# Performance work log

Hardware: AMD Instinct MI355X
Metric: run time of the kernel (lower is better)

The kernel has to match this reference:

```python
import jax, jax.numpy as jnp
import numpy as np

NUM_HEADS = 16
DIM_HEAD = 64
SCALE = DIM_HEAD ** -0.5
ROPE_BASE = 10000.0


def _rope(t):
    # t: [b, h, n, d] -> rotary embedding with rotate-half convention
    n, d = t.shape[2], t.shape[3]
    inv_freq = 1.0 / (ROPE_BASE ** (jnp.arange(0, d, 2, dtype=jnp.float32) / d))
    freqs = jnp.arange(n, dtype=jnp.float32)[:, None] * inv_freq[None, :]  # [n, d/2]
    cos = jnp.concatenate([jnp.cos(freqs), jnp.cos(freqs)], axis=-1)  # [n, d]
    sin = jnp.concatenate([jnp.sin(freqs), jnp.sin(freqs)], axis=-1)
    t1, t2 = jnp.split(t, 2, axis=-1)
    rot = jnp.concatenate([-t2, t1], axis=-1)
    return t * cos + rot * sin


def setup_inputs() -> dict:
    key = jax.random.key(0)
    k1, k2, k3 = jax.random.split(key, 3)
    B, N, D = 2, 2049, 1024  # 2048 patches + 1 cls token
    x = jax.random.normal(k1, (B, N, D), dtype=jnp.float32)
    ln_gamma = jnp.ones((D,), dtype=jnp.float32)
    ln_beta = jnp.zeros((D,), dtype=jnp.float32)
    w_qkv = jax.random.normal(k2, (D, 3 * NUM_HEADS * DIM_HEAD), dtype=jnp.float32) * 0.02
    w_out = jax.random.normal(k3, (NUM_HEADS * DIM_HEAD, D), dtype=jnp.float32) * 0.02
    return {"x": x, "ln_gamma": ln_gamma, "ln_beta": ln_beta, "w_qkv": w_qkv, "w_out": w_out}


def reference(x, ln_gamma, ln_beta, w_qkv, w_out):
    B, N, D = x.shape
    # LayerNorm (eps=1e-5, torch default)
    mu = jnp.mean(x, axis=-1, keepdims=True)
    var = jnp.mean(jnp.square(x - mu), axis=-1, keepdims=True)
    xn = (x - mu) * jax.lax.rsqrt(var + 1e-5) * ln_gamma + ln_beta
    # QKV projection (no bias)
    qkv = xn @ w_qkv  # [B, N, 3*H*Dh]
    q, k, v = jnp.split(qkv, 3, axis=-1)
    def to_heads(t):
        return t.reshape(B, N, NUM_HEADS, DIM_HEAD).transpose(0, 2, 1, 3)  # [B,H,N,Dh]
    q, k, v = to_heads(q), to_heads(k), to_heads(v)
    # cls token excluded from RoPE
    q = jnp.concatenate([q[:, :, :1, :], _rope(q[:, :, 1:, :])], axis=2)
    k = jnp.concatenate([k[:, :, :1, :], _rope(k[:, :, 1:, :])], axis=2)
    dots = jnp.einsum('bhqd,bhkd->bhqk', q, k) * SCALE
    attn = jax.nn.softmax(dots, axis=-1)
    out = jnp.einsum('bhqk,bhkd->bhqd', attn, v)
    out = out.transpose(0, 2, 1, 3).reshape(B, N, NUM_HEADS * DIM_HEAD)
    return out @ w_out
```

## Files before the change

### kernel.cpp

```cpp
#include <hip/hip_runtime.h>

#define B_    2
#define N_    2049
#define NPAD  2112
#define D_    1024
#define H_    16
#define DH    64
#define MROWS (B_ * N_)
#define MPAD  4224
#define QSCALE 0.18033688011117674f

using bf16x8 = __attribute__((ext_vector_type(8))) short;
using f32x4  = __attribute__((ext_vector_type(4))) float;
using f32x16 = __attribute__((ext_vector_type(16))) float;

#define AS1 __attribute__((address_space(1)))
#define AS3 __attribute__((address_space(3)))

__device__ __forceinline__ float bf2f(short s) {
  union { unsigned u; float f; } a; a.u = ((unsigned)(unsigned short)s) << 16; return a.f;
}
__device__ __forceinline__ short f2bf(float f) {
  union { float f; unsigned u; } a; a.f = f;
  unsigned r = a.u + 0x7fffu + ((a.u >> 16) & 1u);
  return (short)(r >> 16);
}
__device__ __forceinline__ float hexp2(float x) { return __builtin_amdgcn_exp2f(x); }
__device__ __forceinline__ void dma16(const short* g, AS3 short* l) {
  __builtin_amdgcn_global_load_lds((const AS1 unsigned*)g, (AS3 unsigned*)l, 16, 0, 0);
}

__device__ __forceinline__ size_t tiled_off(int m, int k) {
  return ((size_t)(m >> 7) << 17)
       + (size_t)(((k >> 5) << 12)
       + ((((m & 127) >> 4)) << 9)
       + (((((m & 15) << 2) | ((k & 31) >> 3))) << 3)
       + (k & 7));
}

__global__ __launch_bounds__(256) void prep_kernel(const float* __restrict__ x,
                                                   const float* __restrict__ gamma,
                                                   const float* __restrict__ beta,
                                                   short* __restrict__ xn,
                                                   const float* __restrict__ w_qkv,
                                                   short* __restrict__ wqkvT,
                                                   const float* __restrict__ w_out,
                                                   short* __restrict__ woutT) {
  int blk = blockIdx.x;
  int tid = threadIdx.x;
  __shared__ float T[64][65];
  __shared__ float sb[4], s2b[4];

  if (blk < MROWS) {
    int row = blk;
    int b = row >= N_;
    int rowp = b * NPAD + (row - b * N_);
    const float4 v = ((const float4*)(x + (size_t)row * D_))[tid];
    float s  = v.x + v.y + v.z + v.w;
    float ss = v.x * v.x + v.y * v.y + v.z * v.z + v.w * v.w;
    for (int o = 1; o < 64; o <<= 1) { s += __shfl_xor(s, o, 64); ss += __shfl_xor(ss, o, 64); }
    int wid = tid >> 6;
    if ((tid & 63) == 0) { sb[wid] = s; s2b[wid] = ss; }
    __syncthreads();
    float st  = sb[0] + sb[1] + sb[2] + sb[3];
    float sst = s2b[0] + s2b[1] + s2b[2] + s2b[3];
    float mu  = st * (1.0f / D_);
    float var = sst * (1.0f / D_) - mu * mu;
    float rs  = rsqrtf(var + 1e-5f);
    const float4 g  = ((const float4*)gamma)[tid];
    const float4 be = ((const float4*)beta)[tid];
    short4 o4;
    o4.x = f2bf((v.x - mu) * rs * g.x + be.x);
    o4.y = f2bf((v.y - mu) * rs * g.y + be.y);
    o4.z = f2bf((v.z - mu) * rs * g.z + be.z);
    o4.w = f2bf((v.w - mu) * rs * g.w + be.w);
    *(short4*)(xn + tiled_off(rowp, tid * 4)) = o4;
    return;
  }

  const float* in; short* out; int Nn, t2;
  int b2 = blk - MROWS;
  if (b2 < 768) { in = w_qkv; out = wqkvT; Nn = 3072; t2 = b2; }
  else          { in = w_out; out = woutT; Nn = 1024; t2 = b2 - 768; }
  int k0 = (t2 & 15) * 64;
  int n0 = (t2 >> 4) * 64;
  int r = tid >> 2, c0 = (tid & 3) * 16;
  const float* ip = in + (size_t)(k0 + r) * Nn + n0 + c0;
  #pragma unroll
  for (int j = 0; j < 4; ++j) {
    float4 v = *(const float4*)(ip + j * 4);
    T[r][c0 + j * 4 + 0] = v.x; T[r][c0 + j * 4 + 1] = v.y;
    T[r][c0 + j * 4 + 2] = v.z; T[r][c0 + j * 4 + 3] = v.w;
  }
  __syncthreads();
  bf16x8 w0, w1;
  #pragma unroll
  for (int j = 0; j < 8; ++j) {
    w0[j] = f2bf(T[c0 + j][r]);
    w1[j] = f2bf(T[c0 + 8 + j][r]);
  }
  *(bf16x8*)(out + tiled_off(n0 + r, k0 + c0))     = w0;
  *(bf16x8*)(out + tiled_off(n0 + r, k0 + c0 + 8)) = w1;
}

#define BM 128
#define BK 32
__global__ __launch_bounds__(256) void gemm_qkv_rope(const short* __restrict__ A,
                                                     const short* __restrict__ BT,
                                                     short* __restrict__ qg,
                                                     short* __restrict__ kfrag,
                                                     short* __restrict__ vfrag) {
  int lane = threadIdx.x & 63, wid = threadIdx.x >> 6;
  int quad = lane >> 4, l16 = lane & 15;
  int wr = wid >> 1, wc = wid & 1;
  int chunk = gridDim.x >> 3;
  int swz = (blockIdx.x & 7) * chunk + (blockIdx.x >> 3);
  int mb = swz % 33, nb = swz / 33;
  int m0 = mb * BM;
  int n0 = nb * BM;

  __shared__ __align__(16) short pool[17408];
  AS3 short* AbufL = (AS3 short*)pool;
  AS3 short* BbufL = (AS3 short*)(pool + 8192);
  const short* AbufR = pool;
  const short* BbufR = pool + 8192;

  f32x4 acc[4][4] = {};

  const short* Ap = A  + ((size_t)(m0 >> 7) << 17);
  const short* Bp = BT + ((size_t)(n0 >> 7) << 17);

  auto stage = [&](int kt, int bb) {
    #pragma unroll
    for (int i = 0; i < 2; ++i) {
      int j = wid * 2 + i;
      dma16(Ap + ((size_t)kt << 12) + j * 512 + lane * 8, AbufL + bb * 4096 + j * 512);
      dma16(Bp + ((size_t)kt << 12) + j * 512 + lane * 8, BbufL + bb * 4096 + j * 512);
    }
  };

  stage(0, 0);
  __syncthreads();

  for (int kt = 0; kt < 32; ++kt) {
    int cur = kt & 1;
    if (kt + 1 < 32) stage(kt + 1, cur ^ 1);
    const short* Ab = AbufR + cur * 4096;
    const short* Bb = BbufR + cur * 4096;
    bf16x8 af[4], bfr[4];
    #pragma unroll
    for (int s = 0; s < 4; ++s)
      af[s] = *(const bf16x8*)&Ab[(wr * 64 + s * 16 + l16) * BK + quad * 8];
    #pragma unroll
    for (int t = 0; t < 4; ++t)
      bfr[t] = *(const bf16x8*)&Bb[(wc * 64 + t * 16 + l16) * BK + quad * 8];
    #pragma unroll
    for (int s = 0; s < 4; ++s)
      #pragma unroll
      for (int t = 0; t < 4; ++t)
        acc[s][t] = __builtin_amdgcn_mfma_f32_16x16x32_bf16(af[s], bfr[t], acc[s][t], 0, 0, 0);
    __syncthreads();
  }

  short* Ct = pool;
  #pragma unroll
  for (int s = 0; s < 4; ++s)
    #pragma unroll
    for (int t = 0; t < 4; ++t) {
      int col = wc * 64 + t * 16 + l16;
      #pragma unroll
      for (int r = 0; r < 4; ++r) {
        int row = wr * 64 + s * 16 + quad * 4 + r;
        Ct[row * 136 + col] = f2bf(acc[s][t][r]);
      }
    }
  __syncthreads();

  int third = nb >> 3;
  int hpair = (nb & 7) * 2;
  int tid = threadIdx.x;

  if (third == 0) {
    int p = tid & 3, nl = tid >> 2;
    #pragma unroll
    for (int tt = 0; tt < 2; ++tt) {
      int rl = tt * 64 + nl;
      int rg = m0 + rl;
      int b = rg >= NPAD;
      int n = rg - b * NPAD;
      bool valid = n < N_;
      bool rot = valid && n > 0;
      float csv[8], snv[8];
      #pragma unroll
      for (int j = 0; j < 8; ++j) {
        int i = p * 8 + j;
        float ang = rot ? (float)(n - 1) * hexp2((float)i * -0.4152410118609203f) : 0.0f;
        float rev = ang * 0.15915494309189535f;
        rev = rev - floorf(rev);
        snv[j] = rot ? __builtin_amdgcn_sinf(rev) : 0.0f;
        csv[j] = rot ? __builtin_amdgcn_cosf(rev) : 1.0f;
      }
      #pragma unroll
      for (int hh = 0; hh < 2; ++hh) {
        bf16x8 w1v = {}, w2v = {};
        if (valid) {
          bf16x8 va = *(const bf16x8*)&Ct[rl * 136 + hh * 64 + p * 8];
          bf16x8 vb = *(const bf16x8*)&Ct[rl * 136 + hh * 64 + p * 8 + 32];
          #pragma unroll
          for (int j = 0; j < 8; ++j) {
            float a = bf2f(va[j]), b2 = bf2f(vb[j]);
            w1v[j] = f2bf((a * csv[j] - b2 * snv[j]) * QSCALE);
            w2v[j] = f2bf((b2 * csv[j] + a * snv[j]) * QSCALE);
          }
        }
        size_t ob = ((size_t)(b * 16 + hpair + hh) * NPAD + n) * DH;
        *(bf16x8*)(qg + ob + p * 8)      = w1v;
        *(bf16x8*)(qg + ob + 32 + p * 8) = w2v;
      }
    }
  } else if (third == 1) {
    int rl = tid & 127, hi = tid >> 7;
    int rg = m0 + rl;
    int b = rg >= NPAD;
    int n = rg - b * NPAD;
    bool valid = n < N_;
    bool rot = valid && n > 0;
    int kt = n >> 6, g = (n >> 5) & 1, lk = n & 31;
    int l = hi * 32 + lk;
    #pragma unroll
    for (int s2 = 0; s2 < 2; ++s2) {
      float csv[8], snv[8];
      #pragma unroll
      for (int j = 0; j < 8; ++j) {
        int i = s2 * 16 + hi * 8 + j;
        float ang = rot ? (float)(n - 1) * hexp2((float)i * -0.4152410118609203f) : 0.0f;
        float rev = ang * 0.15915494309189535f;
        rev = rev - floorf(rev);
        snv[j] = rot ? __builtin_amdgcn_sinf(rev) : 0.0f;
        csv[j] = rot ? __builtin_amdgcn_cosf(rev) : 1.0f;
      }
      #pragma unroll
      for (int hh = 0; hh < 2; ++hh) {
        bf16x8 wlo = {}, whi = {};
        if (valid) {
          bf16x8 va = *(const bf16x8*)&Ct[rl * 136 + hh * 64 + s2 * 16 + hi * 8];
          bf16x8 vb = *(const bf16x8*)&Ct[rl * 136 + hh * 64 + s2 * 16 + hi * 8 + 32];
          #pragma unroll
          for (int j = 0; j < 8; ++j) {
            float a = bf2f(va[j]), b2 = bf2f(vb[j]);
            wlo[j] = f2bf(a * csv[j] - b2 * snv[j]);
            whi[j] = f2bf(b2 * csv[j] + a * snv[j]);
          }
        }
        short* base = kfrag + (size_t)(b * 16 + hpair + hh) * NPAD * DH + (size_t)kt * 4096;
        *(bf16x8*)(base + (g * 4 + s2) * 512 + l * 8)     = wlo;
        *(bf16x8*)(base + (g * 4 + s2 + 2) * 512 + l * 8) = whi;
      }
    }
  } else {
    int lk = tid & 31, z = tid >> 5;
    #pragma unroll
    for (int oo = 0; oo < 2; ++oo) {
      int o = z * 2 + oo;
      int rg = m0 + o * 8;
      int b = rg >= NPAD;
      int n0o = rg - b * NPAD;
      int kt = n0o >> 6;
      int s = (n0o >> 4) & 3;
      int hi = (n0o >> 3) & 1;
      #pragma unroll
      for (int hh = 0; hh < 2; ++hh) {
        short* base = vfrag + (size_t)(b * 16 + hpair + hh) * NPAD * DH + (size_t)kt * 4096;
        #pragma unroll
        for (int m = 0; m < 2; ++m) {
          bf16x8 wv = {};
          #pragma unroll
          for (int j = 0; j < 8; ++j)
            if (n0o + j < N_) wv[j] = Ct[(o * 8 + j) * 136 + hh * 64 + m * 32 + lk];
          *(bf16x8*)(base + (m * 4 + s) * 512 + (hi * 32 + lk) * 8) = wv;
        }
      }
    }
  }
}

template <typename OutT>
__global__ __launch_bounds__(256) void gemm128(const short* __restrict__ A,
                                               const short* __restrict__ BT,
                                               OutT* __restrict__ C,
                                               int Mstore, int Ncols, int K) {
  int lane = threadIdx.x & 63, wid = threadIdx.x >> 6;
  int quad = lane >> 4, l16 = lane & 15;
  int wr = wid >> 1, wc = wid & 1;
  int chunk = gridDim.x >> 3;
  int swz = (blockIdx.x & 7) * chunk + (blockIdx.x >> 3);
  int mb = swz % 33, nb = swz / 33;
  int m0 = mb * BM;
  int n0 = nb * BM;

  __shared__ __align__(16) short Abuf[2][BM * BK];
  __shared__ __align__(16) short Bbuf[2][BM * BK];
  AS3 short* AbufL = (AS3 short*)&Abuf[0][0];
  AS3 short* BbufL = (AS3 short*)&Bbuf[0][0];

  f32x4 acc[4][4] = {};

  const short* Ap = A  + ((size_t)(m0 >> 7) << 17);
  const short* Bp = BT + ((size_t)(n0 >> 7) << 17);

  auto stage = [&](int kt, int bb) {
    #pragma unroll
    for (int i = 0; i < 2; ++i) {
      int j = wid * 2 + i;
      dma16(Ap + ((size_t)kt << 12) + j * 512 + lane * 8, AbufL + bb * (BM * BK) + j * 512);
      dma16(Bp + ((size_t)kt << 12) + j * 512 + lane * 8, BbufL + bb * (BM * BK) + j * 512);
    }
  };

  stage(0, 0);
  __syncthreads();

  int KT = K / BK;
  for (int kt = 0; kt < KT; ++kt) {
    int cur = kt & 1;
    if (kt + 1 < KT) stage(kt + 1, cur ^ 1);
    const short* Ab = &Abuf[cur][0];
    const short* Bb = &Bbuf[cur][0];
    bf16x8 af[4], bfr[4];
    #pragma unroll
    for (int s = 0; s < 4; ++s)
      af[s] = *(const bf16x8*)&Ab[(wr * 64 + s * 16 + l16) * BK + quad * 8];
    #pragma unroll
    for (int t = 0; t < 4; ++t)
      bfr[t] = *(const bf16x8*)&Bb[(wc * 64 + t * 16 + l16) * BK + quad * 8];
    #pragma unroll
    for (int s = 0; s < 4; ++s)
      #pragma unroll
      for (int t = 0; t < 4; ++t)
        acc[s][t] = __builtin_amdgcn_mfma_f32_16x16x32_bf16(af[s], bfr[t], acc[s][t], 0, 0, 0);
    __syncthreads();
  }

  #pragma unroll
  for (int s = 0; s < 4; ++s)
    #pragma unroll
    for (int r = 0; r < 4; ++r) {
      int row = m0 + wr * 64 + s * 16 + quad * 4 + r;
      if (row < Mstore) {
        size_t rb = (size_t)row * Ncols + n0 + wc * 64;
        #pragma unroll
        for (int t = 0; t < 4; ++t) {
          float val = acc[s][t][r];
          if constexpr (sizeof(OutT) == 2)
            C[rb + t * 16 + l16] = (OutT)(unsigned short)f2bf(val);
          else
            C[rb + t * 16 + l16] = (OutT)val;
        }
      }
    }
}

__global__ __launch_bounds__(256, 3) void attn_kernel(const short* __restrict__ qg,
                                                      const short* __restrict__ kfrag,
                                                      const short* __restrict__ vfrag,
                                                      short* __restrict__ out) {
  int blk = blockIdx.x;
  int xcd = blk & 7;
  int t_  = blk >> 3;
  int bh  = xcd * 4 + (t_ & 3);
  int qblk = t_ >> 2;
  int b = bh >> 4, h = bh & 15;

  int lane = threadIdx.x & 63, wid = threadIdx.x >> 6;
  int q    = lane & 31;
  int half = lane >> 5;
  int q0   = qblk * 128 + wid * 32;
  size_t hb = (size_t)bh * NPAD * DH;
  const short* kf_hb = kfrag + hb;
  const short* vf_hb = vfrag + hb;

  __shared__ __align__(16) short Kbuf[3][4096];
  __shared__ __align__(16) short Vbuf[3][4096];
  AS3 short* KbufL = (AS3 short*)&Kbuf[0][0];
  AS3 short* VbufL = (AS3 short*)&Vbuf[0][0];
  const short* KbufR = &Kbuf[0][0];
  const short* VbufR = &Vbuf[0][0];

  int qr = q0 + q; if (qr >= NPAD) qr = 0;
  const short* qp = qg + hb + (size_t)qr * DH + half * 8;
  bf16x8 qf[4];
  #pragma unroll
  for (int s = 0; s < 4; ++s) qf[s] = *(const bf16x8*)(qp + s * 16);

  f32x16 o0 = {}, o1 = {};
  float lrun = 0.0f;

  auto stage = [&](int kt, int bb) {
    const short* ksrc = kf_hb + (size_t)kt * 4096;
    const short* vsrc = vf_hb + (size_t)kt * 4096;
    #pragma unroll
    for (int i = 0; i < 2; ++i) {
      int j = wid * 2 + i;
      dma16(ksrc + j * 512 + lane * 8, KbufL + bb * 4096 + j * 512);
      dma16(vsrc + j * 512 + lane * 8, VbufL + bb * 4096 + j * 512);
    }
  };

  stage(0, 0);
  stage(1, 1);

  #define NKT 33
  for (int kt = 0; kt < NKT; ++kt) {
    int rb = kt % 3;
    int k0 = kt * 64;

    if (kt == NKT - 1) asm volatile("s_waitcnt vmcnt(0)" ::: "memory");
    else               asm volatile("s_waitcnt vmcnt(4)" ::: "memory");
    __builtin_amdgcn_s_barrier();

    if (kt + 2 < NKT) stage(kt + 2, (kt + 2) % 3);
    __builtin_amdgcn_sched_barrier(0);

    const short* Vc = VbufR + rb * 4096;
    bf16x8 vf0[4], vf1[4];
    #pragma unroll
    for (int s = 0; s < 4; ++s) {
      vf0[s] = *(const bf16x8*)&Vc[(0 * 4 + s) * 512 + lane * 8];
      vf1[s] = *(const bf16x8*)&Vc[(4 + s) * 512 + lane * 8];
    }

    const short* Kc = KbufR + rb * 4096;
    f32x16 sA = {}, sB = {};
    __builtin_amdgcn_s_setprio(1);
    #pragma unroll
    for (int s = 0; s < 4; ++s) {
      bf16x8 kf0 = *(const bf16x8*)&Kc[(0 * 4 + s) * 512 + lane * 8];
      bf16x8 kf1 = *(const bf16x8*)&Kc[(1 * 4 + s) * 512 + lane * 8];
      sA = __builtin_amdgcn_mfma_f32_32x32x16_bf16(kf0, qf[s], sA, 0, 0, 0);
      sB = __builtin_amdgcn_mfma_f32_32x32x16_bf16(kf1, qf[s], sB, 0, 0, 0);
    }
    __builtin_amdgcn_s_setprio(0);

    if (k0 + 64 > N_) {
      #pragma unroll
      for (int rr = 0; rr < 16; ++rr) {
        int key = (rr & 3) + 8 * (rr >> 2) + 4 * half;
        if (k0 + key >= N_)      sA[rr] = -1e30f;
        if (k0 + 32 + key >= N_) sB[rr] = -1e30f;
      }
    }

    float vsum = 0.0f;
    #pragma unroll
    for (int rr = 0; rr < 16; ++rr) {
      sA[rr] = hexp2(sA[rr]); vsum += sA[rr];
      sB[rr] = hexp2(sB[rr]); vsum += sB[rr];
    }
    lrun += vsum;

    unsigned w[4][4];
    #pragma unroll
    for (int g = 0; g < 2; ++g) {
      #pragma unroll
      for (int fs = 0; fs < 2; ++fs) {
        int b0 = fs * 8;
        float e0, e1, e2, e3, e4, e5, e6, e7;
        if (g == 0) {
          e0 = sA[b0+0]; e1 = sA[b0+1]; e2 = sA[b0+2]; e3 = sA[b0+3];
          e4 = sA[b0+4]; e5 = sA[b0+5]; e6 = sA[b0+6]; e7 = sA[b0+7];
        } else {
          e0 = sB[b0+0]; e1 = sB[b0+1]; e2 = sB[b0+2]; e3 = sB[b0+3];
          e4 = sB[b0+4]; e5 = sB[b0+5]; e6 = sB[b0+6]; e7 = sB[b0+7];
        }
        unsigned X1, X2, Y1, Y2;
        asm("v_cvt_pk_bf16_f32 %0, %1, %2" : "=v"(X1) : "v"(e0), "v"(e1));
        asm("v_cvt_pk_bf16_f32 %0, %1, %2" : "=v"(X2) : "v"(e2), "v"(e3));
        asm("v_cvt_pk_bf16_f32 %0, %1, %2" : "=v"(Y1) : "v"(e4), "v"(e5));
        asm("v_cvt_pk_bf16_f32 %0, %1, %2" : "=v"(Y2) : "v"(e6), "v"(e7));
        asm("v_permlane32_swap_b32 %0, %1" : "+v"(X1), "+v"(Y1));
        asm("v_permlane32_swap_b32 %0, %1" : "+v"(X2), "+v"(Y2));
        int kst = g * 2 + fs;
        w[kst][0] = X1; w[kst][1] = X2; w[kst][2] = Y1; w[kst][3] = Y2;
      }
    }

    __builtin_amdgcn_s_setprio(1);
    #pragma unroll
    for (int kst = 0; kst < 4; ++kst) {
      union { unsigned u[4]; bf16x8 v; } bw;
      bw.u[0] = w[kst][0]; bw.u[1] = w[kst][1]; bw.u[2] = w[kst][2]; bw.u[3] = w[kst][3];
      o0 = __builtin_amdgcn_mfma_f32_32x32x16_bf16(vf0[kst], bw.v, o0, 0, 0, 0);
      o1 = __builtin_amdgcn_mfma_f32_32x32x16_bf16(vf1[kst], bw.v, o1, 0, 0, 0);
    }
    __builtin_amdgcn_s_setprio(0);
  }

  lrun += __shfl_xor(lrun, 32, 64);

  int qrow = q0 + q;
  if (qrow < N_) {
    float inv = 1.0f / lrun;
    int grow = b * N_ + qrow;
    #pragma unroll
    for (int m = 0; m < 2; ++m) {
      #pragma unroll
      for (int gq = 0; gq < 4; ++gq) {
        float a0 = (m ? o1[gq*4+0] : o0[gq*4+0]) * inv;
        float a1 = (m ? o1[gq*4+1] : o0[gq*4+1]) * inv;
        float a2 = (m ? o1[gq*4+2] : o0[gq*4+2]) * inv;
        float a3 = (m ? o1[gq*4+3] : o0[gq*4+3]) * inv;
        short4 st;
        st.x = f2bf(a0); st.y = f2bf(a1); st.z = f2bf(a2); st.w = f2bf(a3);
        int dh = m * 32 + gq * 8 + half * 4;
        *(short4*)(out + tiled_off(grow, h * DH + dh)) = st;
      }
    }
  }
}

extern "C" void kernel_launch(void* const* d_in, const int* in_sizes, int n_in,
                              void* d_out, int out_size, void* d_ws, size_t ws_size,
                              hipStream_t stream) {
  const float* x     = (const float*)d_in[0];
  const float* gamma = (const float*)d_in[1];
  const float* beta  = (const float*)d_in[2];
  const float* w_qkv = (const float*)d_in[3];
  const float* w_out = (const float*)d_in[4];

  short* wqkvT = (short*)d_ws;
  short* woutT = wqkvT + (size_t)3072 * 1024;
  short* xn    = woutT + (size_t)1024 * 1024;
  short* qg    = xn    + (size_t)MPAD * 1024;
  short* kfragG = qg    + (size_t)B_ * H_ * NPAD * DH;
  short* vfragG = kfragG + (size_t)B_ * H_ * NPAD * DH;
  short* attn_out = xn;

  prep_kernel<<<MROWS + 768 + 256, 256, 0, stream>>>(x, gamma, beta, xn,
                                                     w_qkv, wqkvT, w_out, woutT);
  gemm_qkv_rope<<<792, 256, 0, stream>>>(xn, wqkvT, qg, kfragG, vfragG);
  attn_kernel<<<544, 256, 0, stream>>>(qg, kfragG, vfragG, attn_out);
  gemm128<float><<<264, 256, 0, stream>>>(attn_out, woutT, (float*)d_out, MROWS, 1024, 1024);
}
```

Before: 209.9 us.

## Halve attention and out-projection tile sizes to double block counts

The attention kernel now uses 2-wave blocks covering 64 queries each (1056 blocks instead of 544), and drops from triple to double buffering of K/V tiles with a full vmcnt(0) wait each step. The output projection becomes a specialized 64x128-tile GEMM with 528 blocks instead of 264 blocks of 128x128. Both changes aim to fill the GPU's compute units better and cut tail imbalance. In exchange, K/V reuse per block drops, so more global/L2 traffic, and the shallower prefetch pipeline may expose load latency.

```diff
diff --git a/kernel.cpp b/kernel.cpp
--- a/kernel.cpp
+++ b/kernel.cpp
@@ -284,57 +284,55 @@
   }
 }
 
-template <typename OutT>
-__global__ __launch_bounds__(256) void gemm128(const short* __restrict__ A,
-                                               const short* __restrict__ BT,
-                                               OutT* __restrict__ C,
-                                               int Mstore, int Ncols, int K) {
+__global__ __launch_bounds__(256) void gemm_out(const short* __restrict__ A,
+                                                const short* __restrict__ BT,
+                                                float* __restrict__ C) {
   int lane = threadIdx.x & 63, wid = threadIdx.x >> 6;
   int quad = lane >> 4, l16 = lane & 15;
   int wr = wid >> 1, wc = wid & 1;
   int chunk = gridDim.x >> 3;
   int swz = (blockIdx.x & 7) * chunk + (blockIdx.x >> 3);
-  int mb = swz % 33, nb = swz / 33;
-  int m0 = mb * BM;
-  int n0 = nb * BM;
-
-  __shared__ __align__(16) short Abuf[2][BM * BK];
-  __shared__ __align__(16) short Bbuf[2][BM * BK];
+  int mb = swz % 66, nb = swz / 66;
+  int m0 = mb * 64;
+  int n0 = nb * 128;
+
+  __shared__ __align__(16) short Abuf[2][2048];
+  __shared__ __align__(16) short Bbuf[2][4096];
   AS3 short* AbufL = (AS3 short*)&Abuf[0][0];
   AS3 short* BbufL = (AS3 short*)&Bbuf[0][0];
 
-  f32x4 acc[4][4] = {};
+  f32x4 acc[2][4] = {};
 
   const short* Ap = A  + ((size_t)(m0 >> 7) << 17);
   const short* Bp = BT + ((size_t)(n0 >> 7) << 17);
+  int jbA = (m0 & 127) >> 4;
 
   auto stage = [&](int kt, int bb) {
+    dma16(Ap + ((size_t)kt << 12) + (jbA + wid) * 512 + lane * 8, AbufL + bb * 2048 + wid * 512);
     #pragma unroll
     for (int i = 0; i < 2; ++i) {
       int j = wid * 2 + i;
-      dma16(Ap + ((size_t)kt << 12) + j * 512 + lane * 8, AbufL + bb * (BM * BK) + j * 512);
-      dma16(Bp + ((size_t)kt << 12) + j * 512 + lane * 8, BbufL + bb * (BM * BK) + j * 512);
+      dma16(Bp + ((size_t)kt << 12) + j * 512 + lane * 8, BbufL + bb * 4096 + j * 512);
     }
   };
 
   stage(0, 0);
   __syncthreads();
 
-  int KT = K / BK;
-  for (int kt = 0; kt < KT; ++kt) {
+  for (int kt = 0; kt < 32; ++kt) {
     int cur = kt & 1;
-    if (kt + 1 < KT) stage(kt + 1, cur ^ 1);
+    if (kt + 1 < 32) stage(kt + 1, cur ^ 1);
     const short* Ab = &Abuf[cur][0];
     const short* Bb = &Bbuf[cur][0];
-    bf16x8 af[4], bfr[4];
-    #pragma unroll
-    for (int s = 0; s < 4; ++s)
-      af[s] = *(const bf16x8*)&Ab[(wr * 64 + s * 16 + l16) * BK + quad * 8];
+    bf16x8 af[2], bfr[4];
+    #pragma unroll
+    for (int s = 0; s < 2; ++s)
+      af[s] = *(const bf16x8*)&Ab[(wr * 32 + s * 16 + l16) * BK + quad * 8];
     #pragma unroll
     for (int t = 0; t < 4; ++t)
       bfr[t] = *(const bf16x8*)&Bb[(wc * 64 + t * 16 + l16) * BK + quad * 8];
     #pragma unroll
-    for (int s = 0; s < 4; ++s)
+    for (int s = 0; s < 2; ++s)
       #pragma unroll
       for (int t = 0; t < 4; ++t)
         acc[s][t] = __builtin_amdgcn_mfma_f32_16x16x32_bf16(af[s], bfr[t], acc[s][t], 0, 0, 0);
@@ -342,28 +340,23 @@
   }
 
   #pragma unroll
-  for (int s = 0; s < 4; ++s)
+  for (int s = 0; s < 2; ++s)
     #pragma unroll
     for (int r = 0; r < 4; ++r) {
-      int row = m0 + wr * 64 + s * 16 + quad * 4 + r;
-      if (row < Mstore) {
-        size_t rb = (size_t)row * Ncols + n0 + wc * 64;
+      int row = m0 + wr * 32 + s * 16 + quad * 4 + r;
+      if (row < MROWS) {
+        size_t rb = (size_t)row * 1024 + n0 + wc * 64;
         #pragma unroll
-        for (int t = 0; t < 4; ++t) {
-          float val = acc[s][t][r];
-          if constexpr (sizeof(OutT) == 2)
-            C[rb + t * 16 + l16] = (OutT)(unsigned short)f2bf(val);
-          else
-            C[rb + t * 16 + l16] = (OutT)val;
-        }
-      }
-    }
-}
-
-__global__ __launch_bounds__(256, 3) void attn_kernel(const short* __restrict__ qg,
-                                                      const short* __restrict__ kfrag,
-                                                      const short* __restrict__ vfrag,
-                                                      short* __restrict__ out) {
+        for (int t = 0; t < 4; ++t)
+          C[rb + t * 16 + l16] = acc[s][t][r];
+      }
+    }
+}
+
+__global__ __launch_bounds__(128) void attn_kernel(const short* __restrict__ qg,
+                                                   const short* __restrict__ kfrag,
+                                                   const short* __restrict__ vfrag,
+                                                   short* __restrict__ out) {
   int blk = blockIdx.x;
   int xcd = blk & 7;
   int t_  = blk >> 3;
@@ -374,19 +367,19 @@
   int lane = threadIdx.x & 63, wid = threadIdx.x >> 6;
   int q    = lane & 31;
   int half = lane >> 5;
-  int q0   = qblk * 128 + wid * 32;
+  int q0   = qblk * 64 + wid * 32;
   size_t hb = (size_t)bh * NPAD * DH;
   const short* kf_hb = kfrag + hb;
   const short* vf_hb = vfrag + hb;
 
-  __shared__ __align__(16) short Kbuf[3][4096];
-  __shared__ __align__(16) short Vbuf[3][4096];
+  __shared__ __align__(16) short Kbuf[2][4096];
+  __shared__ __align__(16) short Vbuf[2][4096];
   AS3 short* KbufL = (AS3 short*)&Kbuf[0][0];
   AS3 short* VbufL = (AS3 short*)&Vbuf[0][0];
   const short* KbufR = &Kbuf[0][0];
   const short* VbufR = &Vbuf[0][0];
 
-  int qr = q0 + q; if (qr >= NPAD) qr = 0;
+  int qr = q0 + q;
   const short* qp = qg + hb + (size_t)qr * DH + half * 8;
   bf16x8 qf[4];
   #pragma unroll
@@ -399,26 +392,24 @@
     const short* ksrc = kf_hb + (size_t)kt * 4096;
     const short* vsrc = vf_hb + (size_t)kt * 4096;
     #pragma unroll
-    for (int i = 0; i < 2; ++i) {
-      int j = wid * 2 + i;
+    for (int i = 0; i < 4; ++i) {
+      int j = wid * 4 + i;
       dma16(ksrc + j * 512 + lane * 8, KbufL + bb * 4096 + j * 512);
       dma16(vsrc + j * 512 + lane * 8, VbufL + bb * 4096 + j * 512);
     }
   };
 
   stage(0, 0);
-  stage(1, 1);
 
   #define NKT 33
   for (int kt = 0; kt < NKT; ++kt) {
-    int rb = kt % 3;
+    int rb = kt & 1;
     int k0 = kt * 64;
 
-    if (kt == NKT - 1) asm volatile("s_waitcnt vmcnt(0)" ::: "memory");
-    else               asm volatile("s_waitcnt vmcnt(4)" ::: "memory");
+    asm volatile("s_waitcnt vmcnt(0)" ::: "memory");
     __builtin_amdgcn_s_barrier();
 
-    if (kt + 2 < NKT) stage(kt + 2, (kt + 2) % 3);
+    if (kt + 1 < NKT) stage(kt + 1, rb ^ 1);
     __builtin_amdgcn_sched_barrier(0);
 
     const short* Vc = VbufR + rb * 4096;
@@ -538,6 +529,6 @@
   prep_kernel<<<MROWS + 768 + 256, 256, 0, stream>>>(x, gamma, beta, xn,
                                                      w_qkv, wqkvT, w_out, woutT);
   gemm_qkv_rope<<<792, 256, 0, stream>>>(xn, wqkvT, qg, kfragG, vfragG);
-  attn_kernel<<<544, 256, 0, stream>>>(qg, kfragG, vfragG, attn_out);
-  gemm128<float><<<264, 256, 0, stream>>>(attn_out, woutT, (float*)d_out, MROWS, 1024, 1024);
-}
+  attn_kernel<<<1056, 128, 0, stream>>>(qg, kfragG, vfragG, attn_out);
+  gemm_out<<<528, 256, 0, stream>>>(attn_out, woutT, (float*)d_out);
+}
```

New measurement: 225.9 us. 1.08x slower.
